# Kernel optimization log

Measured on AMD Instinct MI355X. Metric: run time of the kernel, lower is better.

Reference implementation:

```python
import jax, jax.numpy as jnp
import numpy as np

N = 50000          # nodes
E = 400000         # raw edges (doubled to 2E inside forward)
NODE_IN, NODE_OUT = 256, 128
EDGE_IN, EDGE_OUT = 128, 128
ALPHA = 0.2        # LeakyReLU negative slope


def _xavier_uniform(k, shape, gain=1.0):
    limit = gain * np.sqrt(6.0 / (shape[0] + shape[1]))
    return jax.random.uniform(k, shape, jnp.float32, -limit, limit)


def setup_inputs() -> dict:
    key = jax.random.key(0)
    k1, k2, k3, k4, k5, k6 = jax.random.split(key, 6)
    node_fts = jax.random.normal(k1, (N, NODE_IN), jnp.float32)
    edge_fts = jax.random.normal(k2, (E, EDGE_IN), jnp.float32)
    # edges: [1, 2, E]; ensure every node id appears somewhere in the flat
    # tensor so that after doubling+flip every node is a source segment.
    rng = np.random.default_rng(0)
    flat = np.concatenate([np.arange(N), rng.integers(0, N, 2 * E - N)])
    rng.shuffle(flat)
    edges = jnp.asarray(flat.reshape(1, 2, E), dtype=jnp.int32)
    W_node = _xavier_uniform(k3, (NODE_IN, NODE_OUT))
    W_edge = _xavier_uniform(k4, (EDGE_IN, EDGE_OUT))
    a_node = _xavier_uniform(k5, (2 * NODE_OUT, 1), gain=1.414)
    a_edge = _xavier_uniform(k6, (NODE_OUT + EDGE_OUT, 1), gain=1.414)
    return {"node_fts": node_fts, "edge_fts": edge_fts, "edges": edges,
            "W_node": W_node, "W_edge": W_edge,
            "a_node": a_node, "a_edge": a_edge}


def _leaky(x):
    return jnp.where(x >= 0, x, ALPHA * x)


def reference(node_fts, edge_fts, edges, W_node, W_edge, a_node, a_edge):
    ef = jnp.concatenate([edge_fts, edge_fts], axis=0)            # [2E, edge_in]
    # squeeze -> [2,E]; reshape(E,2) is a raw row-major reshape (as in torch)
    e = edges.reshape(E, 2)
    e_all = jnp.concatenate([e, e[:, ::-1]], axis=0)              # [2E, 2]
    src, dst = e_all[:, 0], e_all[:, 1]

    h_v = node_fts @ W_node                                       # [N, dout]
    e_v = ef @ W_edge                                             # [2E, eout]

    h_exp = h_v[e_all].reshape(-1, 2 * NODE_OUT)                  # [2E, 2*dout]
    e_exp = jnp.concatenate([h_v[src], e_v], axis=1)              # [2E, dout+eout]

    natt = jnp.exp(jnp.clip(_leaky((h_exp @ a_node)[:, 0]), -2.0, 2.0))
    eatt = jnp.exp(jnp.clip(_leaky((e_exp @ a_edge)[:, 0]), -2.0, 2.0))

    counts = jnp.bincount(src, length=N)                          # [N]
    nsum = jax.ops.segment_sum(natt, src, num_segments=N)         # [N]
    esum = jax.ops.segment_sum(eatt, src, num_segments=N)         # [N]
    # repeat_interleave(sum, bincount) semantics, positional as in torch
    ndenom = jnp.repeat(nsum, counts, total_repeat_length=2 * E)
    edenom = jnp.repeat(esum, counts, total_repeat_length=2 * E)
    nnorm = natt / ndenom
    enorm = eatt / edenom
    nvar = jnp.var(nnorm, ddof=1)   # torch.var default is unbiased
    evar = jnp.var(enorm, ddof=1)

    node_out = jax.ops.segment_sum(h_v[dst] * nnorm[:, None], src, num_segments=N)
    edge_out = jax.ops.segment_sum(e_v[dst] * enorm[:, None], src, num_segments=N)
    return node_out, edge_out, nvar, evar
```

## Files before the change

### kernel.cpp

```cpp
#include <hip/hip_runtime.h>
#include <hip/hip_bf16.h>

#define NN 50000
#define EE 400000
#define REPS 16
#define QSCALE 131072.0f
#define SCAN_CHUNK 2048

typedef short bf16x8 __attribute__((ext_vector_type(8)));
typedef float f32x4 __attribute__((ext_vector_type(4)));

__device__ inline unsigned bf16pair(float a, float b) {
    unsigned ua = __float_as_uint(a), ub = __float_as_uint(b);
    ua = (ua + 0x7FFFu + ((ua >> 16) & 1u)) >> 16;
    ub = (ub + 0x7FFFu + ((ub >> 16) & 1u)) >> 16;
    return ua | (ub << 16);
}

__global__ void zero_ws(unsigned long long* __restrict__ p, size_t n64) {
    size_t i = (size_t)blockIdx.x * blockDim.x + threadIdx.x;
    size_t stride = (size_t)gridDim.x * blockDim.x;
    for (; i < n64; i += stride) p[i] = 0ULL;
}

__global__ void prep(const float* __restrict__ W_node, const float* __restrict__ W_edge,
                     const float* __restrict__ a_node, const float* __restrict__ a_edge,
                     float* wn_a1, float* wn_a2, float* wn_e1, float* we_a2,
                     unsigned short* __restrict__ Wt_node, unsigned short* __restrict__ Wt_edge) {
    int t = threadIdx.x;
    if (blockIdx.x == 0) {
        if (t < 256) {
            float x1 = 0.f, x2 = 0.f, x3 = 0.f;
            for (int j = 0; j < 128; ++j) {
                float w = W_node[t * 128 + j];
                x1 += w * a_node[j];
                x2 += w * a_node[128 + j];
                x3 += w * a_edge[j];
            }
            wn_a1[t] = x1; wn_a2[t] = x2; wn_e1[t] = x3;
        }
        if (t < 128) {
            float x = 0.f;
            for (int j = 0; j < 128; ++j) x += W_edge[t * 128 + j] * a_edge[128 + j];
            we_a2[t] = x;
        }
    }
    int gid = blockIdx.x * blockDim.x + t;
    int nth = gridDim.x * blockDim.x;
    for (int idx = gid; idx < 256 * 128; idx += nth) {
        int r = idx >> 7, c = idx & 127;
        unsigned u = __float_as_uint(W_node[idx]);
        u = (u + 0x7FFFu + ((u >> 16) & 1u)) >> 16;
        Wt_node[c * 256 + r] = (unsigned short)u;
    }
    for (int idx = gid; idx < 128 * 128; idx += nth) {
        int r = idx >> 7, c = idx & 127;
        unsigned u = __float_as_uint(W_edge[idx]);
        u = (u + 0x7FFFu + ((u >> 16) & 1u)) >> 16;
        Wt_edge[c * 128 + r] = (unsigned short)u;
    }
}

template <int K, int OFFH, bool FUSE3>
__global__ __launch_bounds__(256) void gemm_mfma(const float* __restrict__ A,
                                                 const unsigned short* __restrict__ Wt,
                                                 const float* __restrict__ w1,
                                                 const float* __restrict__ w2,
                                                 const float* __restrict__ w3,
                                                 unsigned* __restrict__ hevu,
                                                 float* __restrict__ o1, float* __restrict__ o2,
                                                 float* __restrict__ o3, int M) {
    int t = threadIdx.x;
    int wv = t >> 6, l = t & 63;
    int rl = l & 15, kg = l >> 4;
    int wrow0 = blockIdx.x * 64 + wv * 16;
    int gr = wrow0 + rl;
    int ar = gr < M ? gr : M - 1;
    const float* Arow = A + (size_t)ar * K;
    f32x4 acc[8];
#pragma unroll
    for (int i = 0; i < 8; ++i) acc[i] = (f32x4){0.f, 0.f, 0.f, 0.f};
    float p1 = 0.f, p2 = 0.f, p3 = 0.f;
    for (int k0 = 0; k0 < K; k0 += 32) {
        int kb = k0 + kg * 8;
        float4 alo = *reinterpret_cast<const float4*>(Arow + kb);
        float4 ahi = *reinterpret_cast<const float4*>(Arow + kb + 4);
        union { unsigned u[4]; bf16x8 v; } af;
        af.u[0] = bf16pair(alo.x, alo.y);
        af.u[1] = bf16pair(alo.z, alo.w);
        af.u[2] = bf16pair(ahi.x, ahi.y);
        af.u[3] = bf16pair(ahi.z, ahi.w);
        if (FUSE3) {
            float4 wl = *reinterpret_cast<const float4*>(w1 + kb);
            float4 wh = *reinterpret_cast<const float4*>(w1 + kb + 4);
            p1 += alo.x * wl.x + alo.y * wl.y + alo.z * wl.z + alo.w * wl.w
                + ahi.x * wh.x + ahi.y * wh.y + ahi.z * wh.z + ahi.w * wh.w;
            wl = *reinterpret_cast<const float4*>(w2 + kb);
            wh = *reinterpret_cast<const float4*>(w2 + kb + 4);
            p2 += alo.x * wl.x + alo.y * wl.y + alo.z * wl.z + alo.w * wl.w
                + ahi.x * wh.x + ahi.y * wh.y + ahi.z * wh.z + ahi.w * wh.w;
        }
        {
            float4 wl = *reinterpret_cast<const float4*>(w3 + kb);
            float4 wh = *reinterpret_cast<const float4*>(w3 + kb + 4);
            p3 += alo.x * wl.x + alo.y * wl.y + alo.z * wl.z + alo.w * wl.w
                + ahi.x * wh.x + ahi.y * wh.y + ahi.z * wh.z + ahi.w * wh.w;
        }
#pragma unroll
        for (int nt = 0; nt < 8; ++nt) {
            union { unsigned u[4]; bf16x8 v; } bf;
            const unsigned* bp = reinterpret_cast<const unsigned*>(Wt + (size_t)(rl + 16 * nt) * K + kb);
            bf.u[0] = bp[0]; bf.u[1] = bp[1]; bf.u[2] = bp[2]; bf.u[3] = bp[3];
            acc[nt] = __builtin_amdgcn_mfma_f32_16x16x32_bf16(af.v, bf.v, acc[nt], 0, 0, 0);
        }
    }
    p3 += __shfl_xor(p3, 16); p3 += __shfl_xor(p3, 32);
    if (FUSE3) {
        p1 += __shfl_xor(p1, 16); p1 += __shfl_xor(p1, 32);
        p2 += __shfl_xor(p2, 16); p2 += __shfl_xor(p2, 32);
        if (l < 16 && gr < M) { o1[gr] = p1; o2[gr] = p2; o3[gr] = p3; }
    } else {
        if (l < 16 && gr < M) o3[gr] = p3;
    }
#pragma unroll
    for (int nt = 0; nt < 8; ++nt) {
#pragma unroll
        for (int reg = 0; reg < 4; ++reg) {
            float mine = acc[nt][reg];
            float other = __shfl_xor(mine, 1);
            int orow = wrow0 + kg * 4 + reg;
            if (orow < M) {
                int col = rl + 16 * nt;
                if (!(l & 1)) {
                    if (reg < 2) hevu[(size_t)orow * 128 + col + OFFH] = bf16pair(mine, other);
                } else {
                    if (reg >= 2) hevu[(size_t)orow * 128 + (col - 1) + OFFH] = bf16pair(other, mine);
                }
            }
        }
    }
}

__global__ void edge_scalar_tail(const float* __restrict__ EF, const float* __restrict__ w,
                                 float* __restrict__ t2e) {
    int wave = NN + (int)((blockIdx.x * (size_t)blockDim.x + threadIdx.x) >> 6);
    int lane = threadIdx.x & 63;
    if (wave >= EE) return;
    float2 v = *reinterpret_cast<const float2*>(EF + (size_t)wave * 128 + lane * 2);
    float a = v.x * w[lane * 2] + v.y * w[lane * 2 + 1];
    for (int off = 32; off; off >>= 1) a += __shfl_down(a, off);
    if (lane == 0) t2e[wave] = a;
}

__global__ void attention(const int* __restrict__ edges, const float* __restrict__ s1,
                          const float* __restrict__ s2, const float* __restrict__ t1,
                          const float* __restrict__ t2e, unsigned long long* __restrict__ histR,
                          unsigned* __restrict__ rank) {
    int i = blockIdx.x * blockDim.x + threadIdx.x;
    if (i >= 2 * EE) return;
    int rep = blockIdx.x & (REPS - 1);
    int s, d, j;
    if (i < EE) { j = i; int2 p = *reinterpret_cast<const int2*>(edges + 2 * j); s = p.x; d = p.y; }
    else        { j = i - EE; int2 p = *reinterpret_cast<const int2*>(edges + 2 * j); s = p.y; d = p.x; }
    float xn = s1[s] + s2[d];
    xn = xn >= 0.f ? xn : 0.2f * xn;
    xn = fminf(fmaxf(xn, -2.f), 2.f);
    float na = expf(xn);
    float xe = t1[s] + t2e[j];
    xe = xe >= 0.f ? xe : 0.2f * xe;
    xe = fminf(fmaxf(xe, -2.f), 2.f);
    float ea = expf(xe);
    unsigned qn = __float2uint_rn(na * QSCALE);
    unsigned qe = __float2uint_rn(ea * QSCALE);
    unsigned long long pk = (1ULL << 56) | ((unsigned long long)qn << 28) | (unsigned long long)qe;
    unsigned long long old = atomicAdd(&histR[(size_t)rep * NN + s], pk);
    rank[i] = (unsigned)(old >> 56);
}

__global__ void reduce_reps(const unsigned long long* __restrict__ histR, float* __restrict__ nsum,
                            float* __restrict__ esum, int* __restrict__ counts,
                            int* __restrict__ bsums) {
    __shared__ int sdata[256];
    int b = blockIdx.x, t = threadIdx.x;
    int base = b * SCAN_CHUNK;
    int csum = 0;
    for (int j = 0; j < 8; ++j) {
        int idx = base + j * 256 + t;
        if (idx < NN) {
            unsigned long long h = 0;
            for (int g = 0; g < REPS; ++g) h += histR[(size_t)g * NN + idx];
            int c = (int)(h >> 56);
            counts[idx] = c;
            nsum[idx] = (float)((h >> 28) & 0x0FFFFFFFULL) * (1.0f / QSCALE);
            esum[idx] = (float)(h & 0x0FFFFFFFULL) * (1.0f / QSCALE);
            csum += c;
        }
    }
    sdata[t] = csum; __syncthreads();
    for (int off = 128; off; off >>= 1) { if (t < off) sdata[t] += sdata[t + off]; __syncthreads(); }
    if (t == 0) bsums[b] = sdata[0];
}

__global__ void scan_bsums(int* __restrict__ bsums, int nb) {
    if (threadIdx.x == 0 && blockIdx.x == 0) {
        int run = 0;
        for (int i = 0; i < nb; ++i) { int v = bsums[i]; bsums[i] = run; run += v; }
    }
}

__global__ void scan_final(const int* __restrict__ counts, const int* __restrict__ bsums,
                           const unsigned long long* __restrict__ histR,
                           int* __restrict__ offsets, int* __restrict__ cursorR,
                           int* __restrict__ g) {
    __shared__ int sdata[256];
    int b = blockIdx.x, t = threadIdx.x;
    int base = b * SCAN_CHUNK + t * 8;
    int loc[8]; int s = 0;
    for (int j = 0; j < 8; ++j) { int idx = base + j; int v = (idx < NN) ? counts[idx] : 0; loc[j] = v; s += v; }
    sdata[t] = s; __syncthreads();
    for (int off = 1; off < 256; off <<= 1) {
        int v = (t >= off) ? sdata[t - off] : 0;
        __syncthreads();
        sdata[t] += v;
        __syncthreads();
    }
    int run = sdata[t] - s + bsums[b];
    for (int j = 0; j < 8; ++j) {
        int idx = base + j;
        if (idx < NN) {
            offsets[idx] = run;
            int r2 = run;
            for (int gg = 0; gg < REPS; ++gg) {
                cursorR[(size_t)gg * NN + idx] = r2;
                r2 += (int)(histR[(size_t)gg * NN + idx] >> 56);
            }
            for (int k = 0; k < loc[j]; ++k) g[run + k] = idx;
            run += loc[j];
        }
    }
}

__global__ void normalize_var(const float* __restrict__ s1, const float* __restrict__ s2,
                              const float* __restrict__ t1, const float* __restrict__ t2e,
                              const float* __restrict__ nsum, const float* __restrict__ esum,
                              const int* __restrict__ g, const int* __restrict__ edges,
                              const int* __restrict__ cursorR, const unsigned* __restrict__ rank,
                              float4* __restrict__ meta, double* __restrict__ acc) {
    int i = blockIdx.x * blockDim.x + threadIdx.x;
    float nn = 0.f, en = 0.f;
    if (i < 2 * EE) {
        int s, d, j;
        if (i < EE) { j = i; int2 p = *reinterpret_cast<const int2*>(edges + 2 * j); s = p.x; d = p.y; }
        else        { j = i - EE; int2 p = *reinterpret_cast<const int2*>(edges + 2 * j); s = p.y; d = p.x; }
        float xn = s1[s] + s2[d];
        xn = xn >= 0.f ? xn : 0.2f * xn;
        xn = fminf(fmaxf(xn, -2.f), 2.f);
        float na = expf(xn);
        float xe = t1[s] + t2e[j];
        xe = xe >= 0.f ? xe : 0.2f * xe;
        xe = fminf(fmaxf(xe, -2.f), 2.f);
        float ea = expf(xe);
        int gi = g[i];
        nn = na / nsum[gi];
        en = ea / esum[gi];
        int rep = (i >> 8) & (REPS - 1);
        int slot = cursorR[(size_t)rep * NN + s] + (int)rank[i];
        meta[slot] = make_float4(__int_as_float(d), nn, en, 0.f);
    }
    double v[4] = { (double)nn, (double)nn * nn, (double)en, (double)en * en };
    __shared__ double sd[4][4];
    int lane = threadIdx.x & 63, wv = threadIdx.x >> 6;
#pragma unroll
    for (int q = 0; q < 4; ++q) {
        double x = v[q];
        for (int off = 32; off; off >>= 1) x += __shfl_down(x, off);
        if (lane == 0) sd[q][wv] = x;
    }
    __syncthreads();
    if (threadIdx.x < 4) {
        double x = sd[threadIdx.x][0] + sd[threadIdx.x][1] + sd[threadIdx.x][2] + sd[threadIdx.x][3];
        atomicAdd(&acc[threadIdx.x], x);
    }
}

__global__ void accumulate(const float4* __restrict__ meta, const int* __restrict__ offsets,
                           const int* __restrict__ counts, const uint4* __restrict__ hev,
                           float* __restrict__ node_out, float* __restrict__ edge_out) {
    int wave = (int)((blockIdx.x * (size_t)blockDim.x + threadIdx.x) >> 6);
    int lane = threadIdx.x & 63;
    if (wave >= NN) return;
    int half = lane >> 5, sl = lane & 31;
    int o = offsets[wave], c = counts[wave];
    float aH0 = 0.f, aH1 = 0.f, aH2 = 0.f, aH3 = 0.f;
    float aE0 = 0.f, aE1 = 0.f, aE2 = 0.f, aE3 = 0.f;
    float4 z = make_float4(0.f, 0.f, 0.f, 0.f);
    uint4 zu = make_uint4(0u, 0u, 0u, 0u);
    int np = (c + 1) >> 1;
    float4 m0 = (half < c) ? meta[o + half] : z;
    uint4 v0 = (half < c) ? hev[(size_t)__float_as_int(m0.x) * 32 + sl] : zu;
    for (int k2 = 0; k2 < np; ++k2) {
        int keN = 2 * (k2 + 1) + half;
        float4 m1 = (keN < c) ? meta[o + keN] : z;
        uint4 v1 = (keN < c) ? hev[(size_t)__float_as_int(m1.x) * 32 + sl] : zu;
        float nn = m0.y, en = m0.z;
        aH0 += __uint_as_float(v0.x << 16) * nn;
        aH1 += __uint_as_float(v0.x & 0xFFFF0000u) * nn;
        aE0 += __uint_as_float(v0.y << 16) * en;
        aE1 += __uint_as_float(v0.y & 0xFFFF0000u) * en;
        aH2 += __uint_as_float(v0.z << 16) * nn;
        aH3 += __uint_as_float(v0.z & 0xFFFF0000u) * nn;
        aE2 += __uint_as_float(v0.w << 16) * en;
        aE3 += __uint_as_float(v0.w & 0xFFFF0000u) * en;
        m0 = m1; v0 = v1;
    }
    aH0 += __shfl_xor(aH0, 32); aH1 += __shfl_xor(aH1, 32);
    aH2 += __shfl_xor(aH2, 32); aH3 += __shfl_xor(aH3, 32);
    aE0 += __shfl_xor(aE0, 32); aE1 += __shfl_xor(aE1, 32);
    aE2 += __shfl_xor(aE2, 32); aE3 += __shfl_xor(aE3, 32);
    if (half == 0) {
        float4 rn = { aH0, aH1, aH2, aH3 };
        float4 re = { aE0, aE1, aE2, aE3 };
        *reinterpret_cast<float4*>(node_out + (size_t)wave * 128 + sl * 4) = rn;
        *reinterpret_cast<float4*>(edge_out + (size_t)wave * 128 + sl * 4) = re;
    }
}

__global__ void finalize_var(const double* __restrict__ acc, float* __restrict__ out_var) {
    if (threadIdx.x == 0 && blockIdx.x == 0) {
        double M = 2.0 * EE;
        double nv = (acc[1] - acc[0] * acc[0] / M) / (M - 1.0);
        double ev = (acc[3] - acc[2] * acc[2] / M) / (M - 1.0);
        out_var[0] = (float)nv;
        out_var[1] = (float)ev;
    }
}

extern "C" void kernel_launch(void* const* d_in, const int* in_sizes, int n_in,
                              void* d_out, int out_size, void* d_ws, size_t ws_size,
                              hipStream_t stream) {
    const float* node_fts = (const float*)d_in[0];
    const float* edge_fts = (const float*)d_in[1];
    const int*   edges    = (const int*)d_in[2];
    const float* W_node   = (const float*)d_in[3];
    const float* W_edge   = (const float*)d_in[4];
    const float* a_node   = (const float*)d_in[5];
    const float* a_edge   = (const float*)d_in[6];
    float* out = (float*)d_out;

    char* w = (char*)d_ws;
    auto alloc = [&](size_t bytes) -> void* {
        void* p = (void*)w;
        w += (bytes + 255) & ~(size_t)255;
        return p;
    };
    unsigned* hevu = (unsigned*)alloc((size_t)NN * 512);
    float* s1    = (float*)alloc(NN * 4);
    float* s2    = (float*)alloc(NN * 4);
    float* t1    = (float*)alloc(NN * 4);
    float* t2e   = (float*)alloc(EE * 4);
    unsigned* rank = (unsigned*)alloc((size_t)2 * EE * 4);
    float4* meta = (float4*)alloc((size_t)2 * EE * 16);
    int*   offsets = (int*)alloc((NN + 1) * 4);
    int*   g       = (int*)alloc(2 * EE * 4);
    int*   bsums   = (int*)alloc(64 * 4);
    float* wn_a1 = (float*)alloc(256 * 4);
    float* wn_a2 = (float*)alloc(256 * 4);
    float* wn_e1 = (float*)alloc(256 * 4);
    float* we_a2 = (float*)alloc(128 * 4);
    unsigned short* Wt_node = (unsigned short*)alloc(256 * 128 * 2);
    unsigned short* Wt_edge = (unsigned short*)alloc(128 * 128 * 2);
    float* nsum   = (float*)alloc(NN * 4);
    float* esum   = (float*)alloc(NN * 4);
    int*   counts = (int*)alloc(NN * 4);
    int*   cursorR = (int*)alloc((size_t)REPS * NN * 4);
    char* zb = (char*)alloc((size_t)REPS * NN * 8 + 64);
    unsigned long long* histR = (unsigned long long*)zb;
    double* acc = (double*)(zb + (size_t)REPS * NN * 8);

    const size_t n64 = (size_t)REPS * NN + 8;
    zero_ws<<<(int)((n64 + 255) / 256), 256, 0, stream>>>((unsigned long long*)zb, n64);

    prep<<<64, 256, 0, stream>>>(W_node, W_edge, a_node, a_edge, wn_a1, wn_a2, wn_e1, we_a2,
                                 Wt_node, Wt_edge);

    const int gemm_grid = (NN + 63) / 64;
    gemm_mfma<256, 0, true><<<gemm_grid, 256, 0, stream>>>(node_fts, Wt_node, wn_a1, wn_a2, wn_e1,
                                                           hevu, s1, s2, t1, NN);
    gemm_mfma<128, 1, false><<<gemm_grid, 256, 0, stream>>>(edge_fts, Wt_edge, nullptr, nullptr,
                                                            we_a2, hevu, nullptr, nullptr, t2e, NN);

    edge_scalar_tail<<<((EE - NN) + 3) / 4, 256, 0, stream>>>(edge_fts, we_a2, t2e);

    attention<<<(2 * EE + 255) / 256, 256, 0, stream>>>(edges, s1, s2, t1, t2e, histR, rank);

    const int nscan = (NN + SCAN_CHUNK - 1) / SCAN_CHUNK;
    reduce_reps<<<nscan, 256, 0, stream>>>(histR, nsum, esum, counts, bsums);
    scan_bsums<<<1, 64, 0, stream>>>(bsums, nscan);
    scan_final<<<nscan, 256, 0, stream>>>(counts, bsums, histR, offsets, cursorR, g);

    normalize_var<<<(2 * EE + 255) / 256, 256, 0, stream>>>(s1, s2, t1, t2e, nsum, esum, g, edges,
                                                            cursorR, rank, meta, acc);

    accumulate<<<(NN + 3) / 4, 256, 0, stream>>>(meta, offsets, counts, (const uint4*)hevu,
                                                 out, out + (size_t)NN * 128);

    finalize_var<<<1, 64, 0, stream>>>(acc, out + (size_t)2 * NN * 128);
}
```

Baseline: 360.0 us.

## Fuse node/edge GEMMs, drop replicated histograms, deepen accumulate prefetch

Merges the node and edge GEMM kernels into one pass that writes both bf16 halves with a single 8-byte store per row/column pair. The 16-way replicated atomic histogram and its per-replica cursors go away, so all edges atomically add into a single per-node histogram and slots come straight from the offsets. The change also switches expf to __expf, adds nontemporal loads and stores for streaming data, and deepens the software prefetch in the accumulate loop. Fewer launches and less histogram traffic are traded against more atomic contention on hot nodes, plus slightly lower exp accuracy.

After: 355.2 us. No clear change (-1.4%).

```diff
diff --git a/kernel.cpp b/kernel.cpp
--- a/kernel.cpp
+++ b/kernel.cpp
@@ -3,12 +3,13 @@
 
 #define NN 50000
 #define EE 400000
-#define REPS 16
 #define QSCALE 131072.0f
 #define SCAN_CHUNK 2048
 
 typedef short bf16x8 __attribute__((ext_vector_type(8)));
 typedef float f32x4 __attribute__((ext_vector_type(4)));
+typedef float f32x4v __attribute__((ext_vector_type(4)));
+typedef float f32x2v __attribute__((ext_vector_type(2)));
 
 __device__ inline unsigned bf16pair(float a, float b) {
     unsigned ua = __float_as_uint(a), ub = __float_as_uint(b);
@@ -61,80 +62,114 @@
     }
 }
 
-template <int K, int OFFH, bool FUSE3>
-__global__ __launch_bounds__(256) void gemm_mfma(const float* __restrict__ A,
-                                                 const unsigned short* __restrict__ Wt,
-                                                 const float* __restrict__ w1,
-                                                 const float* __restrict__ w2,
-                                                 const float* __restrict__ w3,
-                                                 unsigned* __restrict__ hevu,
-                                                 float* __restrict__ o1, float* __restrict__ o2,
-                                                 float* __restrict__ o3, int M) {
+__global__ __launch_bounds__(256) void gemm_fused(const float* __restrict__ NF,
+                                                  const float* __restrict__ EF,
+                                                  const unsigned short* __restrict__ WtN,
+                                                  const unsigned short* __restrict__ WtE,
+                                                  const float* __restrict__ w1,
+                                                  const float* __restrict__ w2,
+                                                  const float* __restrict__ w3,
+                                                  const float* __restrict__ w4,
+                                                  unsigned* __restrict__ hevu,
+                                                  float* __restrict__ s1, float* __restrict__ s2,
+                                                  float* __restrict__ t1, float* __restrict__ t2e,
+                                                  int M) {
     int t = threadIdx.x;
     int wv = t >> 6, l = t & 63;
     int rl = l & 15, kg = l >> 4;
     int wrow0 = blockIdx.x * 64 + wv * 16;
     int gr = wrow0 + rl;
     int ar = gr < M ? gr : M - 1;
-    const float* Arow = A + (size_t)ar * K;
-    f32x4 acc[8];
-#pragma unroll
-    for (int i = 0; i < 8; ++i) acc[i] = (f32x4){0.f, 0.f, 0.f, 0.f};
-    float p1 = 0.f, p2 = 0.f, p3 = 0.f;
-    for (int k0 = 0; k0 < K; k0 += 32) {
+    const float* ArowN = NF + (size_t)ar * 256;
+    const float* ArowE = EF + (size_t)ar * 128;
+    f32x4 accH[8], accE[8];
+#pragma unroll
+    for (int i = 0; i < 8; ++i) { accH[i] = (f32x4){0.f,0.f,0.f,0.f}; accE[i] = (f32x4){0.f,0.f,0.f,0.f}; }
+    float p1 = 0.f, p2 = 0.f, p3 = 0.f, p4 = 0.f;
+    for (int k0 = 0; k0 < 256; k0 += 32) {
         int kb = k0 + kg * 8;
-        float4 alo = *reinterpret_cast<const float4*>(Arow + kb);
-        float4 ahi = *reinterpret_cast<const float4*>(Arow + kb + 4);
+        f32x4v alo = __builtin_nontemporal_load(reinterpret_cast<const f32x4v*>(ArowN + kb));
+        f32x4v ahi = __builtin_nontemporal_load(reinterpret_cast<const f32x4v*>(ArowN + kb + 4));
         union { unsigned u[4]; bf16x8 v; } af;
         af.u[0] = bf16pair(alo.x, alo.y);
         af.u[1] = bf16pair(alo.z, alo.w);
         af.u[2] = bf16pair(ahi.x, ahi.y);
         af.u[3] = bf16pair(ahi.z, ahi.w);
-        if (FUSE3) {
+        {
             float4 wl = *reinterpret_cast<const float4*>(w1 + kb);
             float4 wh = *reinterpret_cast<const float4*>(w1 + kb + 4);
-            p1 += alo.x * wl.x + alo.y * wl.y + alo.z * wl.z + alo.w * wl.w
-                + ahi.x * wh.x + ahi.y * wh.y + ahi.z * wh.z + ahi.w * wh.w;
-            wl = *reinterpret_cast<const float4*>(w2 + kb);
-            wh = *reinterpret_cast<const float4*>(w2 + kb + 4);
-            p2 += alo.x * wl.x + alo.y * wl.y + alo.z * wl.z + alo.w * wl.w
-                + ahi.x * wh.x + ahi.y * wh.y + ahi.z * wh.z + ahi.w * wh.w;
+            p1 += alo.x*wl.x + alo.y*wl.y + alo.z*wl.z + alo.w*wl.w
+                + ahi.x*wh.x + ahi.y*wh.y + ahi.z*wh.z + ahi.w*wh.w;
+        }
+        {
+            float4 wl = *reinterpret_cast<const float4*>(w2 + kb);
+            float4 wh = *reinterpret_cast<const float4*>(w2 + kb + 4);
+            p2 += alo.x*wl.x + alo.y*wl.y + alo.z*wl.z + alo.w*wl.w
+                + ahi.x*wh.x + ahi.y*wh.y + ahi.z*wh.z + ahi.w*wh.w;
         }
         {
             float4 wl = *reinterpret_cast<const float4*>(w3 + kb);
             float4 wh = *reinterpret_cast<const float4*>(w3 + kb + 4);
-            p3 += alo.x * wl.x + alo.y * wl.y + alo.z * wl.z + alo.w * wl.w
-                + ahi.x * wh.x + ahi.y * wh.y + ahi.z * wh.z + ahi.w * wh.w;
+            p3 += alo.x*wl.x + alo.y*wl.y + alo.z*wl.z + alo.w*wl.w
+                + ahi.x*wh.x + ahi.y*wh.y + ahi.z*wh.z + ahi.w*wh.w;
         }
 #pragma unroll
         for (int nt = 0; nt < 8; ++nt) {
             union { unsigned u[4]; bf16x8 v; } bf;
-            const unsigned* bp = reinterpret_cast<const unsigned*>(Wt + (size_t)(rl + 16 * nt) * K + kb);
+            const unsigned* bp = reinterpret_cast<const unsigned*>(WtN + (size_t)(rl + 16*nt) * 256 + kb);
             bf.u[0] = bp[0]; bf.u[1] = bp[1]; bf.u[2] = bp[2]; bf.u[3] = bp[3];
-            acc[nt] = __builtin_amdgcn_mfma_f32_16x16x32_bf16(af.v, bf.v, acc[nt], 0, 0, 0);
-        }
-    }
+            accH[nt] = __builtin_amdgcn_mfma_f32_16x16x32_bf16(af.v, bf.v, accH[nt], 0, 0, 0);
+        }
+    }
+    for (int k0 = 0; k0 < 128; k0 += 32) {
+        int kb = k0 + kg * 8;
+        f32x4v alo = __builtin_nontemporal_load(reinterpret_cast<const f32x4v*>(ArowE + kb));
+        f32x4v ahi = __builtin_nontemporal_load(reinterpret_cast<const f32x4v*>(ArowE + kb + 4));
+        union { unsigned u[4]; bf16x8 v; } af;
+        af.u[0] = bf16pair(alo.x, alo.y);
+        af.u[1] = bf16pair(alo.z, alo.w);
+        af.u[2] = bf16pair(ahi.x, ahi.y);
+        af.u[3] = bf16pair(ahi.z, ahi.w);
+        {
+            float4 wl = *reinterpret_cast<const float4*>(w4 + kb);
+            float4 wh = *reinterpret_cast<const float4*>(w4 + kb + 4);
+            p4 += alo.x*wl.x + alo.y*wl.y + alo.z*wl.z + alo.w*wl.w
+                + ahi.x*wh.x + ahi.y*wh.y + ahi.z*wh.z + ahi.w*wh.w;
+        }
+#pragma unroll
+        for (int nt = 0; nt < 8; ++nt) {
+            union { unsigned u[4]; bf16x8 v; } bf;
+            const unsigned* bp = reinterpret_cast<const unsigned*>(WtE + (size_t)(rl + 16*nt) * 128 + kb);
+            bf.u[0] = bp[0]; bf.u[1] = bp[1]; bf.u[2] = bp[2]; bf.u[3] = bp[3];
+            accE[nt] = __builtin_amdgcn_mfma_f32_16x16x32_bf16(af.v, bf.v, accE[nt], 0, 0, 0);
+        }
+    }
+    p1 += __shfl_xor(p1, 16); p1 += __shfl_xor(p1, 32);
+    p2 += __shfl_xor(p2, 16); p2 += __shfl_xor(p2, 32);
     p3 += __shfl_xor(p3, 16); p3 += __shfl_xor(p3, 32);
-    if (FUSE3) {
-        p1 += __shfl_xor(p1, 16); p1 += __shfl_xor(p1, 32);
-        p2 += __shfl_xor(p2, 16); p2 += __shfl_xor(p2, 32);
-        if (l < 16 && gr < M) { o1[gr] = p1; o2[gr] = p2; o3[gr] = p3; }
-    } else {
-        if (l < 16 && gr < M) o3[gr] = p3;
-    }
+    p4 += __shfl_xor(p4, 16); p4 += __shfl_xor(p4, 32);
+    if (l < 16 && gr < M) { s1[gr] = p1; s2[gr] = p2; t1[gr] = p3; t2e[gr] = p4; }
 #pragma unroll
     for (int nt = 0; nt < 8; ++nt) {
 #pragma unroll
         for (int reg = 0; reg < 4; ++reg) {
-            float mine = acc[nt][reg];
-            float other = __shfl_xor(mine, 1);
+            float hm = accH[nt][reg];
+            float ho = __shfl_xor(hm, 1);
+            float em = accE[nt][reg];
+            float eo = __shfl_xor(em, 1);
             int orow = wrow0 + kg * 4 + reg;
             if (orow < M) {
                 int col = rl + 16 * nt;
                 if (!(l & 1)) {
-                    if (reg < 2) hevu[(size_t)orow * 128 + col + OFFH] = bf16pair(mine, other);
+                    if (reg < 2) {
+                        uint2 wv2 = { bf16pair(hm, ho), bf16pair(em, eo) };
+                        *reinterpret_cast<uint2*>(hevu + (size_t)orow * 128 + col) = wv2;
+                    }
                 } else {
-                    if (reg >= 2) hevu[(size_t)orow * 128 + (col - 1) + OFFH] = bf16pair(other, mine);
+                    if (reg >= 2) {
+                        uint2 wv2 = { bf16pair(ho, hm), bf16pair(eo, em) };
+                        *reinterpret_cast<uint2*>(hevu + (size_t)orow * 128 + (col - 1)) = wv2;
+                    }
                 }
             }
         }
@@ -146,7 +181,7 @@
     int wave = NN + (int)((blockIdx.x * (size_t)blockDim.x + threadIdx.x) >> 6);
     int lane = threadIdx.x & 63;
     if (wave >= EE) return;
-    float2 v = *reinterpret_cast<const float2*>(EF + (size_t)wave * 128 + lane * 2);
+    f32x2v v = __builtin_nontemporal_load(reinterpret_cast<const f32x2v*>(EF + (size_t)wave * 128 + lane * 2));
     float a = v.x * w[lane * 2] + v.y * w[lane * 2 + 1];
     for (int off = 32; off; off >>= 1) a += __shfl_down(a, off);
     if (lane == 0) t2e[wave] = a;
@@ -154,32 +189,31 @@
 
 __global__ void attention(const int* __restrict__ edges, const float* __restrict__ s1,
                           const float* __restrict__ s2, const float* __restrict__ t1,
-                          const float* __restrict__ t2e, unsigned long long* __restrict__ histR,
+                          const float* __restrict__ t2e, unsigned long long* __restrict__ hist,
                           unsigned* __restrict__ rank) {
     int i = blockIdx.x * blockDim.x + threadIdx.x;
     if (i >= 2 * EE) return;
-    int rep = blockIdx.x & (REPS - 1);
     int s, d, j;
     if (i < EE) { j = i; int2 p = *reinterpret_cast<const int2*>(edges + 2 * j); s = p.x; d = p.y; }
     else        { j = i - EE; int2 p = *reinterpret_cast<const int2*>(edges + 2 * j); s = p.y; d = p.x; }
     float xn = s1[s] + s2[d];
     xn = xn >= 0.f ? xn : 0.2f * xn;
     xn = fminf(fmaxf(xn, -2.f), 2.f);
-    float na = expf(xn);
+    float na = __expf(xn);
     float xe = t1[s] + t2e[j];
     xe = xe >= 0.f ? xe : 0.2f * xe;
     xe = fminf(fmaxf(xe, -2.f), 2.f);
-    float ea = expf(xe);
+    float ea = __expf(xe);
     unsigned qn = __float2uint_rn(na * QSCALE);
     unsigned qe = __float2uint_rn(ea * QSCALE);
     unsigned long long pk = (1ULL << 56) | ((unsigned long long)qn << 28) | (unsigned long long)qe;
-    unsigned long long old = atomicAdd(&histR[(size_t)rep * NN + s], pk);
+    unsigned long long old = atomicAdd(&hist[s], pk);
     rank[i] = (unsigned)(old >> 56);
 }
 
-__global__ void reduce_reps(const unsigned long long* __restrict__ histR, float* __restrict__ nsum,
-                            float* __restrict__ esum, int* __restrict__ counts,
-                            int* __restrict__ bsums) {
+__global__ void reduce_unpack(const unsigned long long* __restrict__ hist, float* __restrict__ nsum,
+                              float* __restrict__ esum, int* __restrict__ counts,
+                              int* __restrict__ bsums) {
     __shared__ int sdata[256];
     int b = blockIdx.x, t = threadIdx.x;
     int base = b * SCAN_CHUNK;
@@ -187,8 +221,7 @@
     for (int j = 0; j < 8; ++j) {
         int idx = base + j * 256 + t;
         if (idx < NN) {
-            unsigned long long h = 0;
-            for (int g = 0; g < REPS; ++g) h += histR[(size_t)g * NN + idx];
+            unsigned long long h = hist[idx];
             int c = (int)(h >> 56);
             counts[idx] = c;
             nsum[idx] = (float)((h >> 28) & 0x0FFFFFFFULL) * (1.0f / QSCALE);
@@ -209,9 +242,7 @@
 }
 
 __global__ void scan_final(const int* __restrict__ counts, const int* __restrict__ bsums,
-                           const unsigned long long* __restrict__ histR,
-                           int* __restrict__ offsets, int* __restrict__ cursorR,
-                           int* __restrict__ g) {
+                           int* __restrict__ offsets, int* __restrict__ g) {
     __shared__ int sdata[256];
     int b = blockIdx.x, t = threadIdx.x;
     int base = b * SCAN_CHUNK + t * 8;
@@ -229,11 +260,6 @@
         int idx = base + j;
         if (idx < NN) {
             offsets[idx] = run;
-            int r2 = run;
-            for (int gg = 0; gg < REPS; ++gg) {
-                cursorR[(size_t)gg * NN + idx] = r2;
-                r2 += (int)(histR[(size_t)gg * NN + idx] >> 56);
-            }
             for (int k = 0; k < loc[j]; ++k) g[run + k] = idx;
             run += loc[j];
         }
@@ -244,7 +270,7 @@
                               const float* __restrict__ t1, const float* __restrict__ t2e,
                               const float* __restrict__ nsum, const float* __restrict__ esum,
                               const int* __restrict__ g, const int* __restrict__ edges,
-                              const int* __restrict__ cursorR, const unsigned* __restrict__ rank,
+                              const int* __restrict__ offsets, const unsigned* __restrict__ rank,
                               float4* __restrict__ meta, double* __restrict__ acc) {
     int i = blockIdx.x * blockDim.x + threadIdx.x;
     float nn = 0.f, en = 0.f;
@@ -255,16 +281,15 @@
         float xn = s1[s] + s2[d];
         xn = xn >= 0.f ? xn : 0.2f * xn;
         xn = fminf(fmaxf(xn, -2.f), 2.f);
-        float na = expf(xn);
+        float na = __expf(xn);
         float xe = t1[s] + t2e[j];
         xe = xe >= 0.f ? xe : 0.2f * xe;
         xe = fminf(fmaxf(xe, -2.f), 2.f);
-        float ea = expf(xe);
+        float ea = __expf(xe);
         int gi = g[i];
         nn = na / nsum[gi];
         en = ea / esum[gi];
-        int rep = (i >> 8) & (REPS - 1);
-        int slot = cursorR[(size_t)rep * NN + s] + (int)rank[i];
+        int slot = offsets[s] + (int)rank[i];
         meta[slot] = make_float4(__int_as_float(d), nn, en, 0.f);
     }
     double v[4] = { (double)nn, (double)nn * nn, (double)en, (double)en * en };
@@ -296,12 +321,16 @@
     float4 z = make_float4(0.f, 0.f, 0.f, 0.f);
     uint4 zu = make_uint4(0u, 0u, 0u, 0u);
     int np = (c + 1) >> 1;
-    float4 m0 = (half < c) ? meta[o + half] : z;
-    uint4 v0 = (half < c) ? hev[(size_t)__float_as_int(m0.x) * 32 + sl] : zu;
-    for (int k2 = 0; k2 < np; ++k2) {
-        int keN = 2 * (k2 + 1) + half;
-        float4 m1 = (keN < c) ? meta[o + keN] : z;
-        uint4 v1 = (keN < c) ? hev[(size_t)__float_as_int(m1.x) * 32 + sl] : zu;
+    int e0 = half, e1 = 2 + half, e2i = 4 + half;
+    float4 m0 = (e0 < c) ? meta[o + e0] : z;
+    float4 m1 = (e1 < c) ? meta[o + e1] : z;
+    float4 m2 = (e2i < c) ? meta[o + e2i] : z;
+    uint4 v0 = (e0 < c) ? hev[(size_t)__float_as_int(m0.x) * 32 + sl] : zu;
+    uint4 v1 = (e1 < c) ? hev[(size_t)__float_as_int(m1.x) * 32 + sl] : zu;
+    for (int k = 0; k < np; ++k) {
+        int ep2 = 2 * (k + 2) + half, ep3 = 2 * (k + 3) + half;
+        uint4 v2 = (ep2 < c) ? hev[(size_t)__float_as_int(m2.x) * 32 + sl] : zu;
+        float4 m3 = (ep3 < c) ? meta[o + ep3] : z;
         float nn = m0.y, en = m0.z;
         aH0 += __uint_as_float(v0.x << 16) * nn;
         aH1 += __uint_as_float(v0.x & 0xFFFF0000u) * nn;
@@ -311,17 +340,17 @@
         aH3 += __uint_as_float(v0.z & 0xFFFF0000u) * nn;
         aE2 += __uint_as_float(v0.w << 16) * en;
         aE3 += __uint_as_float(v0.w & 0xFFFF0000u) * en;
-        m0 = m1; v0 = v1;
+        m0 = m1; m1 = m2; m2 = m3; v0 = v1; v1 = v2;
     }
     aH0 += __shfl_xor(aH0, 32); aH1 += __shfl_xor(aH1, 32);
     aH2 += __shfl_xor(aH2, 32); aH3 += __shfl_xor(aH3, 32);
     aE0 += __shfl_xor(aE0, 32); aE1 += __shfl_xor(aE1, 32);
     aE2 += __shfl_xor(aE2, 32); aE3 += __shfl_xor(aE3, 32);
     if (half == 0) {
-        float4 rn = { aH0, aH1, aH2, aH3 };
-        float4 re = { aE0, aE1, aE2, aE3 };
-        *reinterpret_cast<float4*>(node_out + (size_t)wave * 128 + sl * 4) = rn;
-        *reinterpret_cast<float4*>(edge_out + (size_t)wave * 128 + sl * 4) = re;
+        f32x4v rn = { aH0, aH1, aH2, aH3 };
+        f32x4v re = { aE0, aE1, aE2, aE3 };
+        __builtin_nontemporal_store(rn, reinterpret_cast<f32x4v*>(node_out + (size_t)wave * 128 + sl * 4));
+        __builtin_nontemporal_store(re, reinterpret_cast<f32x4v*>(edge_out + (size_t)wave * 128 + sl * 4));
     }
 }
 
@@ -372,34 +401,32 @@
     float* nsum   = (float*)alloc(NN * 4);
     float* esum   = (float*)alloc(NN * 4);
     int*   counts = (int*)alloc(NN * 4);
-    int*   cursorR = (int*)alloc((size_t)REPS * NN * 4);
-    char* zb = (char*)alloc((size_t)REPS * NN * 8 + 64);
-    unsigned long long* histR = (unsigned long long*)zb;
-    double* acc = (double*)(zb + (size_t)REPS * NN * 8);
-
-    const size_t n64 = (size_t)REPS * NN + 8;
+    char* zb = (char*)alloc((size_t)NN * 8 + 64);
+    unsigned long long* hist = (unsigned long long*)zb;
+    double* acc = (double*)(zb + (size_t)NN * 8);
+
+    const size_t n64 = (size_t)NN + 8;
     zero_ws<<<(int)((n64 + 255) / 256), 256, 0, stream>>>((unsigned long long*)zb, n64);
 
     prep<<<64, 256, 0, stream>>>(W_node, W_edge, a_node, a_edge, wn_a1, wn_a2, wn_e1, we_a2,
                                  Wt_node, Wt_edge);
 
     const int gemm_grid = (NN + 63) / 64;
-    gemm_mfma<256, 0, true><<<gemm_grid, 256, 0, stream>>>(node_fts, Wt_node, wn_a1, wn_a2, wn_e1,
-                                                           hevu, s1, s2, t1, NN);
-    gemm_mfma<128, 1, false><<<gemm_grid, 256, 0, stream>>>(edge_fts, Wt_edge, nullptr, nullptr,
-                                                            we_a2, hevu, nullptr, nullptr, t2e, NN);
+    gemm_fused<<<gemm_grid, 256, 0, stream>>>(node_fts, edge_fts, Wt_node, Wt_edge,
+                                              wn_a1, wn_a2, wn_e1, we_a2,
+                                              hevu, s1, s2, t1, t2e, NN);
 
     edge_scalar_tail<<<((EE - NN) + 3) / 4, 256, 0, stream>>>(edge_fts, we_a2, t2e);
 
-    attention<<<(2 * EE + 255) / 256, 256, 0, stream>>>(edges, s1, s2, t1, t2e, histR, rank);
+    attention<<<(2 * EE + 255) / 256, 256, 0, stream>>>(edges, s1, s2, t1, t2e, hist, rank);
 
     const int nscan = (NN + SCAN_CHUNK - 1) / SCAN_CHUNK;
-    reduce_reps<<<nscan, 256, 0, stream>>>(histR, nsum, esum, counts, bsums);
+    reduce_unpack<<<nscan, 256, 0, stream>>>(hist, nsum, esum, counts, bsums);
     scan_bsums<<<1, 64, 0, stream>>>(bsums, nscan);
-    scan_final<<<nscan, 256, 0, stream>>>(counts, bsums, histR, offsets, cursorR, g);
+    scan_final<<<nscan, 256, 0, stream>>>(counts, bsums, offsets, g);
 
     normalize_var<<<(2 * EE + 255) / 256, 256, 0, stream>>>(s1, s2, t1, t2e, nsum, esum, g, edges,
-                                                            cursorR, rank, meta, acc);
+                                                            offsets, rank, meta, acc);
 
     accumulate<<<(NN + 3) / 4, 256, 0, stream>>>(meta, offsets, counts, (const uint4*)hevu,
                                                  out, out + (size_t)NN * 128);
```
